# Performance work log

Measured on AMD Instinct MI355X. Metric: run time of the kernel, lower is better.

The kernel has to match this reference:

```python
import jax, jax.numpy as jnp
import numpy as np
from jax import lax

# Static configuration (torch module passes these as shape lists / init kwargs)
RATE = 2
FUSE_K = 3
SOFTMAX_SCALE = 10.0
B, L, C = 1, 4096, 64
HS = WS = 64            # downscaled foreground spatial (int_fs)
HB = WB = 64            # background patch grid (int_bs); HB*WB == L
KP = 2 * RATE           # raw patch kernel size = 4
PAD_T = 1               # torch conv_transpose2d padding


def setup_inputs() -> dict:
    key = jax.random.key(0)
    ks = jax.random.split(key, 6)
    raw_w = jax.random.normal(ks[0], (B, L, C, KP, KP), jnp.float32) * 0.1
    mm = (jax.random.uniform(ks[1], (B, L, 1, 1)) > 0.5).astype(jnp.float32)
    scores = jax.random.normal(ks[2], (B, L, HS, WS), jnp.float32)
    w1 = jax.random.normal(ks[3], (C, C, 3, 3), jnp.float32) * 0.05
    b1 = jnp.zeros((C,), jnp.float32)
    w2 = jax.random.normal(ks[4], (C, C, 3, 3), jnp.float32) * 0.05
    b2 = jnp.zeros((C,), jnp.float32)
    return {"raw_w": raw_w, "mm": mm, "scores": scores,
            "w1": w1, "b1": b1, "w2": w2, "b2": b2}


def _conv2d(x, w, b=None, padding=1):
    y = lax.conv_general_dilated(x, w, (1, 1), [(padding, padding)] * 2,
                                 dimension_numbers=('NCHW', 'OIHW', 'NCHW'))
    if b is not None:
        y = y + b[None, :, None, None]
    return y


def _fuse(yi):
    # Diagonal-kernel fusion (DeepFill): treat scores as a (HB*WB) x (HS*WS) image
    # and convolve with an identity (eye) kernel along both pairings.
    k = FUSE_K
    eye = jnp.eye(k, dtype=yi.dtype)[None, None]  # [1,1,k,k]
    x = yi.reshape(B, 1, HB * WB, HS * WS)
    x = _conv2d(x, eye, padding=k // 2)
    x = x.reshape(B, HB, WB, HS, WS).transpose(0, 2, 1, 4, 3)
    x = x.reshape(B, 1, WB * HB, WS * HS)
    x = _conv2d(x, eye, padding=k // 2)
    x = x.reshape(B, WB, HB, WS, HS).transpose(0, 2, 1, 4, 3)  # [B,HB,WB,HS,WS]
    return x.reshape(B, L, HS, WS)


def _deconv_item(y_b, w_b):
    # torch F.conv_transpose2d(y, w, stride=RATE, padding=PAD_T) for one item.
    # y_b: [L,HS,WS], w_b: [L,C,KP,KP] -> [C, RATE*HS, RATE*WS]
    wt = jnp.flip(w_b, axis=(-2, -1)).transpose(1, 0, 2, 3)  # [C,L,KP,KP]
    pad = KP - 1 - PAD_T
    out = lax.conv_general_dilated(y_b[None], wt, (1, 1), [(pad, pad)] * 2,
                                   lhs_dilation=(RATE, RATE),
                                   dimension_numbers=('NCHW', 'OIHW', 'NCHW'))
    return out[0] / 4.0  # overlap normalization (4 = number of overlapping patches)


def reference(raw_w, mm, scores, w1, b1, w2, b2):
    yi = _fuse(scores)
    yi = jax.nn.softmax(yi * mm * SOFTMAX_SCALE, axis=1) * mm  # softmax over L patches
    y = jax.vmap(_deconv_item)(yi, raw_w)  # [B, C, RATE*HS, RATE*WS]
    # trailing Conv+ELU x2 (self.out)
    y = jax.nn.elu(_conv2d(y, w1, b1))
    y = jax.nn.elu(_conv2d(y, w2, b2))
    return y
```

## Files before the change

kernel.cpp:

```cpp
#include <hip/hip_runtime.h>
#include <hip/hip_bf16.h>
#include <math.h>

#define NL 4096
#define NQ 4096
#define SCALE 10.0f

typedef __bf16 bf16x8 __attribute__((ext_vector_type(8)));
typedef float  f32x4  __attribute__((ext_vector_type(4)));
typedef float  f32x4u __attribute__((ext_vector_type(4), aligned(4)));

#define GLOAD_LDS16(gp, lp)                                                        \
    __builtin_amdgcn_global_load_lds((const __attribute__((address_space(1))) void*)(gp), \
                                     (__attribute__((address_space(3))) void*)(lp), \
                                     16, 0, 0)

__global__ __launch_bounds__(256) void fuseD(const float* __restrict__ S,
                                             float* __restrict__ F) {
    int lin = blockIdx.x;
    int blk = (lin & 7) * 128 + (lin >> 3);
    int l0 = blk * 4;
    int hb = l0 >> 6, wb0 = l0 & 63;
    int tid = threadIdx.x, lane = tid & 63;

    int rowbase[3]; float wm[3][4];
    #pragma unroll
    for (int d = 0; d < 3; ++d) {
        int h2 = hb + d - 1;
        #pragma unroll
        for (int i = 0; i < 4; ++i) wm[d][i] = 1.f;
        if (h2 >= 0 && h2 <= 63) rowbase[d] = h2 * 64 + wb0;
        else if (h2 < 0) {
            rowbase[d] = 4031 + wb0;
            #pragma unroll
            for (int i = 0; i < 4; ++i) wm[d][i] = (wb0 + i >= 1) ? 1.f : 0.f;
        } else {
            rowbase[d] = 1 + wb0;
            #pragma unroll
            for (int i = 0; i < 4; ++i) wm[d][i] = (wb0 + i <= 62) ? 1.f : 0.f;
        }
    }

    for (int cc = 0; cc < 4; ++cc) {
        int q0 = (cc * 256 + tid) * 4;
        int hs = q0 >> 6, ws0 = q0 & 63;
        f32x4 z4 = {0.f, 0.f, 0.f, 0.f};
        f32x4 acc0 = z4, acc1 = z4, acc2 = z4, acc3 = z4;

        #pragma unroll
        for (int d = 0; d < 3; ++d) {
            int s2 = hs + d - 1;
            bool cw = (s2 < 0) || (s2 > 63);
            int colb = cw ? ((s2 < 0 ? 4031 : 1) + ws0) : (q0 + (d - 1) * 64);
            int cb = cw ? colb - 1 : colb;

            f32x4 v[6], v2[6];
            #pragma unroll
            for (int r = 0; r < 6; ++r) {
                int rr = rowbase[d] - 1 + r;
                v[r] = z4;
                if (rr >= 0 && rr < 4096)
                    v[r] = *(const f32x4u*)(S + (size_t)rr * 4096 + cb);
            }
            if (cw) {
                #pragma unroll
                for (int r = 0; r < 6; ++r) {
                    int rr = rowbase[d] - 1 + r;
                    v2[r] = z4;
                    if (rr >= 0 && rr < 4096)
                        v2[r] = *(const f32x4u*)(S + (size_t)rr * 4096 + colb + 1);
                }
            }

            float lm[4], rm[4];
            #pragma unroll
            for (int r = 0; r < 4; ++r) lm[r] = __shfl_up(v[r][3], 1);
            #pragma unroll
            for (int r = 0; r < 4; ++r) rm[r] = __shfl_down(v[r + 2][0], 1);
            if (!cw) {
                if (lane == 0 || colb == 0) {
                    #pragma unroll
                    for (int r = 0; r < 4; ++r) {
                        int rr = rowbase[d] - 1 + r;
                        lm[r] = (colb > 0 && rr >= 0 && rr < 4096)
                                ? S[(size_t)rr * 4096 + colb - 1] : 0.f;
                    }
                }
                if (lane == 63 || colb + 4 >= 4096) {
                    #pragma unroll
                    for (int r = 0; r < 4; ++r) {
                        int rr = rowbase[d] + 1 + r;
                        rm[r] = (colb + 4 < 4096 && rr >= 0 && rr < 4096)
                                ? S[(size_t)rr * 4096 + colb + 4] : 0.f;
                    }
                }
            }

            f32x4 t[4];
            if (!cw) {
                #pragma unroll
                for (int i = 0; i < 4; ++i) {
                    f32x4 Lv = { lm[i], v[i][0], v[i][1], v[i][2] };
                    f32x4 Cv = v[i + 1];
                    f32x4 Rv = { v[i + 2][1], v[i + 2][2], v[i + 2][3], rm[i] };
                    t[i] = Lv + Cv + Rv;
                }
            } else {
                #pragma unroll
                for (int i = 0; i < 4; ++i) {
                    f32x4 Lv = v[i];
                    f32x4 Cv = { v[i+1][1], v[i+1][2], v[i+1][3], v2[i+1][2] };
                    f32x4 Rv = v2[i + 2];
                    t[i] = Lv + Cv + Rv;
                }
                if (s2 < 0 && ws0 == 0) { t[0][0] = 0.f; t[1][0] = 0.f; t[2][0] = 0.f; t[3][0] = 0.f; }
                if (s2 > 63 && ws0 == 60) { t[0][3] = 0.f; t[1][3] = 0.f; t[2][3] = 0.f; t[3][3] = 0.f; }
            }
            acc0 += wm[d][0] * t[0];
            acc1 += wm[d][1] * t[1];
            acc2 += wm[d][2] * t[2];
            acc3 += wm[d][3] * t[3];
        }
        *(f32x4*)(F + (size_t)(l0 + 0) * 4096 + q0) = acc0;
        *(f32x4*)(F + (size_t)(l0 + 1) * 4096 + q0) = acc1;
        *(f32x4*)(F + (size_t)(l0 + 2) * 4096 + q0) = acc2;
        *(f32x4*)(F + (size_t)(l0 + 3) * 4096 + q0) = acc3;
    }
}

__global__ __launch_bounds__(256) void softPart(const float* __restrict__ F,
                                                const float* __restrict__ mm,
                                                float* __restrict__ Pm,
                                                float* __restrict__ Ps) {
    int qt = blockIdx.x, lc = blockIdx.y;
    int qo = threadIdx.x & 63, lg = threadIdx.x >> 6;
    int q = qt * 64 + qo;
    __shared__ float red[4][64];

    float sv[32];
    float m = -1e30f;
    #pragma unroll
    for (int i = 0; i < 32; ++i) {
        int l = lc * 128 + i * 4 + lg;
        float s = F[(size_t)l * 4096 + q] * mm[l] * SCALE;
        sv[i] = s;
        m = fmaxf(m, s);
    }
    red[lg][qo] = m;
    __syncthreads();
    m = fmaxf(fmaxf(red[0][qo], red[1][qo]), fmaxf(red[2][qo], red[3][qo]));
    __syncthreads();

    float sum = 0.f;
    #pragma unroll
    for (int i = 0; i < 32; ++i) sum += __expf(sv[i] - m);
    red[lg][qo] = sum;
    __syncthreads();
    if (lg == 0) {
        sum = red[0][qo] + red[1][qo] + red[2][qo] + red[3][qo];
        Pm[lc * 4096 + q] = m;
        Ps[lc * 4096 + q] = sum;
    }
}

__global__ void softComb(const float* __restrict__ Pm, const float* __restrict__ Ps,
                         float* __restrict__ Qm, float* __restrict__ Qi) {
    int q = blockIdx.x * 256 + threadIdx.x;
    float M = -1e30f;
    #pragma unroll
    for (int i = 0; i < 32; ++i) M = fmaxf(M, Pm[i * 4096 + q]);
    float S = 0.f;
    #pragma unroll
    for (int i = 0; i < 32; ++i) S += Ps[i * 4096 + q] * __expf(Pm[i * 4096 + q] - M);
    Qm[q] = M;
    Qi[q] = 1.0f / S;
}

__global__ __launch_bounds__(256) void normTransP(const float* __restrict__ F,
                                                  const float* __restrict__ mm,
                                                  const float* __restrict__ Qm,
                                                  const float* __restrict__ Qi,
                                                  __hip_bfloat16* __restrict__ Pt) {
    __shared__ float T[64][65];
    int qt = blockIdx.x, lt = blockIdx.y;
    int c = threadIdx.x & 63;
    int q = qt * 64 + c;
    float qm = Qm[q], qi = Qi[q];
    #pragma unroll
    for (int p = 0; p < 16; ++p) {
        int r = p * 4 + (threadIdx.x >> 6);
        int l = lt * 64 + r;
        float mml = mm[l];
        float s = F[(size_t)l * 4096 + q] * mml * SCALE - qm;
        T[r][c] = mml * __expf(s) * qi;
    }
    __syncthreads();
    #pragma unroll
    for (int p = 0; p < 16; ++p) {
        int r = p * 4 + (threadIdx.x >> 6);
        Pt[(size_t)(qt * 64 + r) * 4096 + lt * 64 + c] = (__hip_bfloat16)T[c][r];
    }
}

__global__ __launch_bounds__(256) void transW(const float* __restrict__ Wsrc,
                                              __hip_bfloat16* __restrict__ Wt) {
    __shared__ float T[64][65];
    int nt = blockIdx.x, kt = blockIdx.y;
    int c = threadIdx.x & 63;
    #pragma unroll
    for (int p = 0; p < 16; ++p) {
        int r = p * 4 + (threadIdx.x >> 6);
        T[r][c] = Wsrc[(size_t)(kt * 64 + r) * 1024 + nt * 64 + c];
    }
    __syncthreads();
    #pragma unroll
    for (int p = 0; p < 16; ++p) {
        int r = p * 4 + (threadIdx.x >> 6);
        int n_new = (r & 15) * 64 + nt * 4 + (r >> 4);
        Wt[(size_t)n_new * 4096 + kt * 64 + c] = (__hip_bfloat16)T[c][r];
    }
}

__global__ void transWc(const float* __restrict__ Wsrc, __hip_bfloat16* __restrict__ Wd) {
    int t = blockIdx.x * 256 + threadIdx.x;
    int kyx = t >> 12;
    int co = (t >> 6) & 63;
    int ci = t & 63;
    Wd[t] = (__hip_bfloat16)Wsrc[co * 576 + ci * 9 + kyx];
}

__global__ __launch_bounds__(256) void gemmMfmaK(const __hip_bfloat16* __restrict__ Ab,
                                                 const __hip_bfloat16* __restrict__ Bb,
                                                 float* __restrict__ C0,
                                                 float* __restrict__ C1,
                                                 float* __restrict__ C2,
                                                 float* __restrict__ C3) {
    __shared__ __align__(16) __hip_bfloat16 As[2][128][32];
    __shared__ __align__(16) __hip_bfloat16 Bs[2][128][32];
    int lin = blockIdx.x;
    int wid = (lin & 7) * 128 + (lin >> 3);
    int bz = wid >> 8;
    int r5 = wid & 255;
    int bn = r5 & 7;
    int bm = r5 >> 3;
    int bm0 = bm * 128, bn0 = bn * 128;
    size_t kbase = (size_t)bz * 1024;
    float* Cm = (bz == 0) ? C0 : (bz == 1) ? C1 : (bz == 2) ? C2 : C3;

    int tid = threadIdx.x;
    int lane = tid & 63, w = tid >> 6;
    int wm = (w >> 1) * 64, wn = (w & 1) * 64;

    int srow = w * 32 + (lane >> 2);
    int scol = (((lane & 3) ^ ((lane >> 3) & 3))) * 8;
    const __hip_bfloat16* ga0 = Ab + (size_t)(bm0 + srow) * 4096 + kbase + scol;
    const __hip_bfloat16* ga1 = Ab + (size_t)(bm0 + srow + 16) * 4096 + kbase + scol;
    const __hip_bfloat16* gb0 = Bb + (size_t)(bn0 + srow) * 4096 + kbase + scol;
    const __hip_bfloat16* gb1 = Bb + (size_t)(bn0 + srow + 16) * 4096 + kbase + scol;

    f32x4 acc[4][4] = {};
    int fm = lane & 15;
    int fkz = (((lane >> 4) ^ ((lane >> 1) & 3))) * 8;

    GLOAD_LDS16(ga0, &As[0][w * 32][0]);
    GLOAD_LDS16(ga1, &As[0][w * 32 + 16][0]);
    GLOAD_LDS16(gb0, &Bs[0][w * 32][0]);
    GLOAD_LDS16(gb1, &Bs[0][w * 32 + 16][0]);
    __syncthreads();

    int buf = 0;
    for (int t = 0; t < 32; ++t) {
        if (t + 1 < 32) {
            int k0 = (t + 1) * 32;
            GLOAD_LDS16(ga0 + k0, &As[buf ^ 1][w * 32][0]);
            GLOAD_LDS16(ga1 + k0, &As[buf ^ 1][w * 32 + 16][0]);
            GLOAD_LDS16(gb0 + k0, &Bs[buf ^ 1][w * 32][0]);
            GLOAD_LDS16(gb1 + k0, &Bs[buf ^ 1][w * 32 + 16][0]);
        }
        bf16x8 af[4], bfr[4];
        #pragma unroll
        for (int i = 0; i < 4; ++i)
            af[i] = *(const bf16x8*)&As[buf][wm + i * 16 + fm][fkz];
        #pragma unroll
        for (int j = 0; j < 4; ++j)
            bfr[j] = *(const bf16x8*)&Bs[buf][wn + j * 16 + fm][fkz];
        #pragma unroll
        for (int i = 0; i < 4; ++i)
            #pragma unroll
            for (int j = 0; j < 4; ++j)
                acc[i][j] = __builtin_amdgcn_mfma_f32_16x16x32_bf16(af[i], bfr[j], acc[i][j], 0, 0, 0);
        __syncthreads();
        buf ^= 1;
    }

    #pragma unroll
    for (int i = 0; i < 4; ++i) {
        #pragma unroll
        for (int j = 0; j < 4; ++j) {
            int row = bm0 + wm + i * 16 + (lane >> 4) * 4;
            int col = bn0 + wn + j * 16 + (lane & 15);
            #pragma unroll
            for (int r = 0; r < 4; ++r)
                Cm[(size_t)(row + r) * 1024 + col] = acc[i][j][r];
        }
    }
}

__global__ void scatterD(const float* __restrict__ Mo, const float* __restrict__ Mo2,
                         const float* __restrict__ Mo3, const float* __restrict__ Mo4,
                         __hip_bfloat16* __restrict__ Xp) {
    int c = threadIdx.x & 63;
    int pix = blockIdx.x * 4 + (threadIdx.x >> 6);
    int ox = pix & 127, oy = pix >> 7;
    float acc = 0.f;
    #pragma unroll
    for (int ky = 0; ky < 4; ++ky) {
        int ty = oy + 1 - ky;
        if (ty & 1) continue;
        int iy = ty >> 1;
        if (iy < 0 || iy >= 64) continue;
        #pragma unroll
        for (int kx = 0; kx < 4; ++kx) {
            int txx = ox + 1 - kx;
            if (txx & 1) continue;
            int ix = txx >> 1;
            if (ix < 0 || ix >= 64) continue;
            size_t off = (size_t)(iy * 64 + ix) * 1024 + (ky * 4 + kx) * 64 + c;
            acc += (Mo[off] + Mo2[off]) + (Mo3[off] + Mo4[off]);
        }
    }
    Xp[((size_t)(oy + 1) * 130 + ox + 1) * 64 + c] = (__hip_bfloat16)(acc * 0.25f);
}

template <int MODE>
__global__ __launch_bounds__(256) void convMfma(const __hip_bfloat16* __restrict__ Xp,
                                                const __hip_bfloat16* __restrict__ Wc,
                                                const float* __restrict__ Bi,
                                                __hip_bfloat16* __restrict__ Yp,
                                                float* __restrict__ Yo) {
    int tid = threadIdx.x, lane = tid & 63, w = tid >> 6;
    int y = blockIdx.x >> 1, x0 = (blockIdx.x & 1) * 64;
    int co0 = w * 16;
    int fl = lane & 15, fh = lane >> 4;

    bf16x8 wb[3][3][2];
    #pragma unroll
    for (int ky = 0; ky < 3; ++ky)
        #pragma unroll
        for (int kx = 0; kx < 3; ++kx)
            #pragma unroll
            for (int kc = 0; kc < 2; ++kc)
                wb[ky][kx][kc] = *(const bf16x8*)&Wc[(size_t)((ky * 3 + kx) * 64 + co0 + fl) * 64 + kc * 32 + fh * 8];

    f32x4 acc[4] = {};
    #pragma unroll
    for (int ky = 0; ky < 3; ++ky) {
        #pragma unroll
        for (int kx = 0; kx < 3; ++kx) {
            const __hip_bfloat16* xrow = Xp + ((size_t)(y + ky) * 130 + x0 + kx) * 64;
            #pragma unroll
            for (int kc = 0; kc < 2; ++kc) {
                #pragma unroll
                for (int mt = 0; mt < 4; ++mt) {
                    bf16x8 af = *(const bf16x8*)&xrow[(mt * 16 + fl) * 64 + kc * 32 + fh * 8];
                    acc[mt] = __builtin_amdgcn_mfma_f32_16x16x32_bf16(af, wb[ky][kx][kc], acc[mt], 0, 0, 0);
                }
            }
        }
    }

    float bias = Bi[co0 + fl];
    #pragma unroll
    for (int mt = 0; mt < 4; ++mt) {
        int xb = x0 + mt * 16 + fh * 4;
        if (MODE == 0) {
            #pragma unroll
            for (int r = 0; r < 4; ++r) {
                float v = acc[mt][r] + bias;
                v = v > 0.f ? v : expm1f(v);
                Yp[((size_t)(y + 1) * 130 + xb + r + 1) * 64 + co0 + fl] = (__hip_bfloat16)v;
            }
        } else {
            float4 o;
            float* op = (float*)&o;
            #pragma unroll
            for (int r = 0; r < 4; ++r) {
                float v = acc[mt][r] + bias;
                op[r] = v > 0.f ? v : expm1f(v);
            }
            *(float4*)&Yo[(size_t)(co0 + fl) * 16384 + y * 128 + xb] = o;
        }
    }
}

extern "C" void kernel_launch(void* const* d_in, const int* in_sizes, int n_in,
                              void* d_out, int out_size, void* d_ws, size_t ws_size,
                              hipStream_t stream) {
    const float* raw_w  = (const float*)d_in[0];
    const float* mm     = (const float*)d_in[1];
    const float* scores = (const float*)d_in[2];
    const float* w1     = (const float*)d_in[3];
    const float* b1     = (const float*)d_in[4];
    const float* w2     = (const float*)d_in[5];
    const float* b2     = (const float*)d_in[6];
    float* out = (float*)d_out;

    char* ws = (char*)d_ws;
    __hip_bfloat16* Pt  = (__hip_bfloat16*)ws;
    __hip_bfloat16* Wt  = (__hip_bfloat16*)(ws + (32ull << 20));
    float*          Pm  = (float*)(ws + (40ull << 20));
    float*          Ps  = (float*)(ws + (40ull << 20) + (512u << 10));
    float*          Qm  = (float*)(ws + (41ull << 20));
    float*          Qi  = (float*)(ws + (41ull << 20) + (64u << 10));
    __hip_bfloat16* Wc1 = (__hip_bfloat16*)(ws + (41ull << 20) + (256u << 10));
    __hip_bfloat16* Wc2 = (__hip_bfloat16*)(ws + (41ull << 20) + (384u << 10));
    float*          Mo  = (float*)(ws + (42ull << 20));
    __hip_bfloat16* Xp  = (__hip_bfloat16*)(ws + (58ull << 20));
    __hip_bfloat16* Y1p = (__hip_bfloat16*)(ws + (61ull << 20));
    float*          F   = (float*)(ws + (64ull << 20));
    float*          Mo2 = (float*)(ws + (64ull << 20));
    float*          Mo3 = (float*)(ws + (80ull << 20));
    float*          Mo4 = (float*)(ws + (96ull << 20));

    const size_t XP_BYTES = 130ull * 130 * 64 * sizeof(__hip_bfloat16);

    fuseD<<<1024, 256, 0, stream>>>(scores, F);
    transW<<<dim3(16, 64), 256, 0, stream>>>(raw_w, Wt);
    transWc<<<144, 256, 0, stream>>>(w1, Wc1);
    transWc<<<144, 256, 0, stream>>>(w2, Wc2);
    softPart<<<dim3(64, 32), 256, 0, stream>>>(F, mm, Pm, Ps);
    softComb<<<16, 256, 0, stream>>>(Pm, Ps, Qm, Qi);
    normTransP<<<dim3(64, 64), 256, 0, stream>>>(F, mm, Qm, Qi, Pt);
    gemmMfmaK<<<1024, 256, 0, stream>>>(Pt, Wt, Mo, Mo2, Mo3, Mo4);
    hipMemsetAsync(Xp, 0, XP_BYTES, stream);
    hipMemsetAsync(Y1p, 0, XP_BYTES, stream);
    scatterD<<<4096, 256, 0, stream>>>(Mo, Mo2, Mo3, Mo4, Xp);
    convMfma<0><<<256, 256, 0, stream>>>(Xp, Wc1, b1, Y1p, nullptr);
    convMfma<1><<<256, 256, 0, stream>>>(Y1p, Wc2, b2, nullptr, out);
}
```

Before: 172.6 us.

## Store split-K GEMM partials in fp16 and vectorize normTransP loads/stores

The four split-K GEMM partial outputs are now written as fp16 instead of fp32, which halves the traffic for the GEMM epilogue writes and the scatterD reads, and the workspace layout is repacked to match. normTransP is also rewritten to read F as float4 and write the transposed bf16 output 4 elements at a time, replacing scalar accesses. Storing the partials in fp16 lowers precision and risks overflow or underflow of the intermediate sums.

After: 166.7 us. 1.03x faster.

```diff
diff --git a/kernel.cpp b/kernel.cpp
--- a/kernel.cpp
+++ b/kernel.cpp
@@ -1,5 +1,6 @@
 #include <hip/hip_runtime.h>
 #include <hip/hip_bf16.h>
+#include <hip/hip_fp16.h>
 #include <math.h>
 
 #define NL 4096
@@ -183,22 +184,32 @@
                                                   __hip_bfloat16* __restrict__ Pt) {
     __shared__ float T[64][65];
     int qt = blockIdx.x, lt = blockIdx.y;
-    int c = threadIdx.x & 63;
-    int q = qt * 64 + c;
-    float qm = Qm[q], qi = Qi[q];
-    #pragma unroll
-    for (int p = 0; p < 16; ++p) {
-        int r = p * 4 + (threadIdx.x >> 6);
-        int l = lt * 64 + r;
-        float mml = mm[l];
-        float s = F[(size_t)l * 4096 + q] * mml * SCALE - qm;
-        T[r][c] = mml * __expf(s) * qi;
-    }
-    __syncthreads();
-    #pragma unroll
-    for (int p = 0; p < 16; ++p) {
-        int r = p * 4 + (threadIdx.x >> 6);
-        Pt[(size_t)(qt * 64 + r) * 4096 + lt * 64 + c] = (__hip_bfloat16)T[c][r];
+    int t = threadIdx.x;
+    int lq = t >> 4;
+    int q4 = (t & 15) * 4;
+    float4 qm4 = *(const float4*)&Qm[qt * 64 + q4];
+    float4 qi4 = *(const float4*)&Qi[qt * 64 + q4];
+
+    #pragma unroll
+    for (int p = 0; p < 4; ++p) {
+        int l = p * 16 + lq;
+        float mml = mm[lt * 64 + l];
+        f32x4 v = *(const f32x4*)&F[(size_t)(lt * 64 + l) * 4096 + qt * 64 + q4];
+        T[l][q4 + 0] = mml * __expf(v[0] * mml * SCALE - qm4.x) * qi4.x;
+        T[l][q4 + 1] = mml * __expf(v[1] * mml * SCALE - qm4.y) * qi4.y;
+        T[l][q4 + 2] = mml * __expf(v[2] * mml * SCALE - qm4.z) * qi4.z;
+        T[l][q4 + 3] = mml * __expf(v[3] * mml * SCALE - qm4.w) * qi4.w;
+    }
+    __syncthreads();
+
+    int l4 = (t & 15) * 4;
+    #pragma unroll
+    for (int p = 0; p < 4; ++p) {
+        int ql = p * 16 + (t >> 4);
+        __hip_bfloat16 ob[4];
+        #pragma unroll
+        for (int i = 0; i < 4; ++i) ob[i] = (__hip_bfloat16)T[l4 + i][ql];
+        *(uint2*)&Pt[(size_t)(qt * 64 + ql) * 4096 + lt * 64 + l4] = *(const uint2*)ob;
     }
 }
 
@@ -231,10 +242,10 @@
 
 __global__ __launch_bounds__(256) void gemmMfmaK(const __hip_bfloat16* __restrict__ Ab,
                                                  const __hip_bfloat16* __restrict__ Bb,
-                                                 float* __restrict__ C0,
-                                                 float* __restrict__ C1,
-                                                 float* __restrict__ C2,
-                                                 float* __restrict__ C3) {
+                                                 __half* __restrict__ C0,
+                                                 __half* __restrict__ C1,
+                                                 __half* __restrict__ C2,
+                                                 __half* __restrict__ C3) {
     __shared__ __align__(16) __hip_bfloat16 As[2][128][32];
     __shared__ __align__(16) __hip_bfloat16 Bs[2][128][32];
     int lin = blockIdx.x;
@@ -245,7 +256,7 @@
     int bm = r5 >> 3;
     int bm0 = bm * 128, bn0 = bn * 128;
     size_t kbase = (size_t)bz * 1024;
-    float* Cm = (bz == 0) ? C0 : (bz == 1) ? C1 : (bz == 2) ? C2 : C3;
+    __half* Cm = (bz == 0) ? C0 : (bz == 1) ? C1 : (bz == 2) ? C2 : C3;
 
     int tid = threadIdx.x;
     int lane = tid & 63, w = tid >> 6;
@@ -301,13 +312,13 @@
             int col = bn0 + wn + j * 16 + (lane & 15);
             #pragma unroll
             for (int r = 0; r < 4; ++r)
-                Cm[(size_t)(row + r) * 1024 + col] = acc[i][j][r];
-        }
-    }
-}
-
-__global__ void scatterD(const float* __restrict__ Mo, const float* __restrict__ Mo2,
-                         const float* __restrict__ Mo3, const float* __restrict__ Mo4,
+                Cm[(size_t)(row + r) * 1024 + col] = __float2half(acc[i][j][r]);
+        }
+    }
+}
+
+__global__ void scatterD(const __half* __restrict__ Mo, const __half* __restrict__ Mo2,
+                         const __half* __restrict__ Mo3, const __half* __restrict__ Mo4,
                          __hip_bfloat16* __restrict__ Xp) {
     int c = threadIdx.x & 63;
     int pix = blockIdx.x * 4 + (threadIdx.x >> 6);
@@ -326,7 +337,8 @@
             int ix = txx >> 1;
             if (ix < 0 || ix >= 64) continue;
             size_t off = (size_t)(iy * 64 + ix) * 1024 + (ky * 4 + kx) * 64 + c;
-            acc += (Mo[off] + Mo2[off]) + (Mo3[off] + Mo4[off]);
+            acc += (__half2float(Mo[off]) + __half2float(Mo2[off]))
+                 + (__half2float(Mo3[off]) + __half2float(Mo4[off]));
         }
     }
     Xp[((size_t)(oy + 1) * 130 + ox + 1) * 64 + c] = (__hip_bfloat16)(acc * 0.25f);
@@ -414,13 +426,13 @@
     float*          Qi  = (float*)(ws + (41ull << 20) + (64u << 10));
     __hip_bfloat16* Wc1 = (__hip_bfloat16*)(ws + (41ull << 20) + (256u << 10));
     __hip_bfloat16* Wc2 = (__hip_bfloat16*)(ws + (41ull << 20) + (384u << 10));
-    float*          Mo  = (float*)(ws + (42ull << 20));
+    __half*         Mo  = (__half*)(ws + (42ull << 20));
+    __half*         Mo2 = (__half*)(ws + (50ull << 20));
     __hip_bfloat16* Xp  = (__hip_bfloat16*)(ws + (58ull << 20));
     __hip_bfloat16* Y1p = (__hip_bfloat16*)(ws + (61ull << 20));
     float*          F   = (float*)(ws + (64ull << 20));
-    float*          Mo2 = (float*)(ws + (64ull << 20));
-    float*          Mo3 = (float*)(ws + (80ull << 20));
-    float*          Mo4 = (float*)(ws + (96ull << 20));
+    __half*         Mo3 = (__half*)(ws + (64ull << 20));
+    __half*         Mo4 = (__half*)(ws + (72ull << 20));
 
     const size_t XP_BYTES = 130ull * 130 * 64 * sizeof(__hip_bfloat16);
 
```
